# Performance work log

Hardware: AMD Instinct MI355X
Metric: run time of the kernel (lower is better)

Reference implementation:

```python
import jax, jax.numpy as jnp
import numpy as np

N_NODES = 50000
N_EDGES = 800000
D = 128


def setup_inputs() -> dict:
    key = jax.random.key(0)
    k1, k2, k3, k4 = jax.random.split(key, 4)
    x = jax.random.normal(k1, (N_NODES, D), dtype=jnp.float32)
    # nn.Linear(in, out, bias=False) weight: [out, in]
    W = jax.random.normal(k2, (D, D), dtype=jnp.float32) / np.sqrt(D)
    src = jax.random.randint(k3, (N_EDGES,), 0, N_NODES, dtype=jnp.int64)
    dst = jax.random.randint(k4, (N_EDGES,), 0, N_NODES, dtype=jnp.int64)
    return {"x": x, "W": W, "src": src, "dst": dst}


def reference(x, W, src, dst):
    # copy_src + reduce_sum: sum incoming neighbor features per destination node
    agg = jax.ops.segment_sum(x[src], dst, num_segments=N_NODES)  # [N, D]
    h = agg @ W.T                      # linear, no bias
    h = jax.nn.relu(h)                 # dropout is identity in eval mode
    h = h + x                          # residual (is_normalize=False)
    return h
```

## Files before the change

### kernel.cpp

```cpp
#include <hip/hip_runtime.h>

#define N_NODES 50000
#define N_EDGES 800000
#define D 128

#define P1_BLOCKS 64
#define P1_GRID   512
#define EDGES_PER_BLOCK (N_EDGES / P1_BLOCKS)
#define EPB_ITERS 13
#define BIN_NODES 32
#define N_BINS 1564
#define CHUNK_CAP 31
#define CELL_WORDS 32
#define LIST_CAP 48
#define RS 136

#define WS_WB16   0
#define WS_SORTED 8192
#define WS_XBF16  3211264
#define WS_END_SORT ((size_t)(WS_XBF16 + 3200000) * 4)

#define NB_SCAN ((N_NODES + 255) / 256)
#define WS_CNT     0
#define WS_ROWPTR  50000
#define WS_BSUMS   100352
#define WS_SRCS    100608
#define WS_END_CSR ((size_t)(WS_SRCS + N_EDGES) * 4)

using bf16x8 = __attribute__((ext_vector_type(8))) short;
using f32x4  = __attribute__((ext_vector_type(4))) float;

__device__ __forceinline__ unsigned bf16rne(float f) {
    unsigned b = __float_as_uint(f);
    return (b + 0x7fffu + ((b >> 16) & 1u)) >> 16;
}

__device__ __forceinline__ uint4 pack8(float4 a, float4 b) {
    uint4 o;
    o.x = bf16rne(a.x) | (bf16rne(a.y) << 16);
    o.y = bf16rne(a.z) | (bf16rne(a.w) << 16);
    o.z = bf16rne(b.x) | (bf16rne(b.y) << 16);
    o.w = bf16rne(b.z) | (bf16rne(b.w) << 16);
    return o;
}

__global__ __launch_bounds__(1024) void p1_convert_partition_kernel(
    const float* __restrict__ x, const float* __restrict__ W,
    const int* __restrict__ src, const int* __restrict__ dst,
    uint4* __restrict__ xb, uint4* __restrict__ wb,
    unsigned* __restrict__ sorted)
{
    const int tid = threadIdx.x;
    const int bid = blockIdx.x;

    if (bid >= P1_BLOCKS) {
        const int gid = (bid - P1_BLOCKS) * 1024 + tid;
        const int stride = (P1_GRID - P1_BLOCKS) * 1024;
        const float4* x4 = (const float4*)x;
        for (int i = gid; i < (N_NODES * D) / 8; i += stride)
            xb[i] = pack8(x4[2 * i], x4[2 * i + 1]);
        const float4* W4 = (const float4*)W;
        for (int i = gid; i < (D * D) / 8; i += stride)
            wb[i] = pack8(W4[2 * i], W4[2 * i + 1]);
        return;
    }

    __shared__ int lhist[N_BINS];
    for (int b = tid; b < N_BINS; b += 1024) lhist[b] = 0;
    __syncthreads();

    const int e0 = bid * EDGES_PER_BLOCK;
    int dd[EPB_ITERS], ss[EPB_ITERS];
    #pragma unroll
    for (int k = 0; k < EPB_ITERS; ++k) {
        int i = k * 1024 + tid;
        if (i < EDGES_PER_BLOCK) {
            dd[k] = dst[e0 + i];
            ss[k] = src[e0 + i];
        } else {
            dd[k] = -1;
            ss[k] = 0;
        }
    }
    #pragma unroll
    for (int k = 0; k < EPB_ITERS; ++k) {
        int d = dd[k];
        if (d >= 0) {
            int bin = d >> 5;
            int pos = atomicAdd(&lhist[bin], 1);
            if (pos < CHUNK_CAP)
                sorted[(size_t)(bin * P1_BLOCKS + bid) * CELL_WORDS + 1 + pos] =
                    ((unsigned)(d & 31) << 16) | ((unsigned)ss[k] & 0xffffu);
        }
    }
    __syncthreads();
    for (int b = tid; b < N_BINS; b += 1024)
        sorted[(size_t)(b * P1_BLOCKS + bid) * CELL_WORDS] = (unsigned)lhist[b];
}

__device__ __forceinline__ void acc_u4(float* acc, uint4 v)
{
    acc[0] += __uint_as_float(v.x << 16);
    acc[1] += __uint_as_float(v.x & 0xffff0000u);
    acc[2] += __uint_as_float(v.y << 16);
    acc[3] += __uint_as_float(v.y & 0xffff0000u);
    acc[4] += __uint_as_float(v.z << 16);
    acc[5] += __uint_as_float(v.z & 0xffff0000u);
    acc[6] += __uint_as_float(v.w << 16);
    acc[7] += __uint_as_float(v.w & 0xffff0000u);
}

__global__ __launch_bounds__(512) void gather_gemm_kernel(
    const uint4* __restrict__ xb, const unsigned* __restrict__ sorted,
    const unsigned short* __restrict__ Wb, float* __restrict__ out)
{
    __shared__ unsigned short list[BIN_NODES * LIST_CAP];
    __shared__ int lcnt[BIN_NODES];
    __shared__ unsigned short Ab[BIN_NODES * RS];
    const int tid = threadIdx.x;
    const int bin = blockIdx.x;
    if (tid < BIN_NODES) lcnt[tid] = 0;
    __syncthreads();

    {
        const int ch = tid >> 3;
        const int sub = tid & 7;
        const unsigned* base = sorted + (size_t)(bin * P1_BLOCKS + ch) * CELL_WORDS;
        int cc = (int)base[0];
        if (cc > CHUNK_CAP) cc = CHUNK_CAP;
        for (int i = sub; i < cc; i += 8) {
            unsigned p = base[1 + i];
            int dl = p >> 16;
            int pos = atomicAdd(&lcnt[dl], 1);
            if (pos < LIST_CAP) list[dl * LIST_CAP + pos] = (unsigned short)(p & 0xffffu);
        }
    }
    __syncthreads();

    {
        const int nl = tid >> 4;
        const int lane = tid & 15;
        int cc = lcnt[nl];
        if (cc > LIST_CAP) cc = LIST_CAP;
        const unsigned short* bk = &list[nl * LIST_CAP];

        float acc[8];
        #pragma unroll
        for (int i = 0; i < 8; ++i) acc[i] = 0.f;
        int e = 0;
        for (; e + 8 <= cc; e += 8) {
            uint4 v[8];
            #pragma unroll
            for (int j = 0; j < 8; ++j) v[j] = xb[(int)bk[e + j] * 16 + lane];
            #pragma unroll
            for (int j = 0; j < 8; ++j) acc_u4(acc, v[j]);
        }
        for (; e + 4 <= cc; e += 4) {
            uint4 v0 = xb[(int)bk[e] * 16 + lane];
            uint4 v1 = xb[(int)bk[e + 1] * 16 + lane];
            uint4 v2 = xb[(int)bk[e + 2] * 16 + lane];
            uint4 v3 = xb[(int)bk[e + 3] * 16 + lane];
            acc_u4(acc, v0); acc_u4(acc, v1); acc_u4(acc, v2); acc_u4(acc, v3);
        }
        for (; e < cc; ++e) acc_u4(acc, xb[(int)bk[e] * 16 + lane]);

        unsigned short* arow = &Ab[nl * RS + lane * 8];
        #pragma unroll
        for (int i = 0; i < 8; ++i) arow[i] = (unsigned short)bf16rne(acc[i]);
    }
    __syncthreads();

    const int wv = tid >> 6;
    const int lane64 = tid & 63;
    const int m = lane64 & 15;
    const int quad = lane64 >> 4;
    const int rt = wv >> 2;

    bf16x8 afrag[4];
    #pragma unroll
    for (int s = 0; s < 4; ++s)
        afrag[s] = *(const bf16x8*)(&Ab[(rt * 16 + m) * RS + quad * 8 + s * 32]);

    const unsigned short* xbs = (const unsigned short*)xb;

    #pragma unroll
    for (int half = 0; half < 2; ++half) {
        const int ct = (wv & 3) * 2 + half;
        f32x4 acc = {0.f, 0.f, 0.f, 0.f};
        const unsigned short* wrow = Wb + (size_t)(ct * 16 + m) * D + quad * 8;
        #pragma unroll
        for (int s = 0; s < 4; ++s) {
            bf16x8 bfrag = *(const bf16x8*)(wrow + s * 32);
            acc = __builtin_amdgcn_mfma_f32_16x16x32_bf16(afrag[s], bfrag, acc, 0, 0, 0);
        }
        const int cc2 = ct * 16 + m;
        #pragma unroll
        for (int r = 0; r < 4; ++r) {
            int rr = bin * BIN_NODES + rt * 16 + quad * 4 + r;
            if (rr < N_NODES) {
                float xf = __uint_as_float((unsigned)xbs[(size_t)rr * D + cc2] << 16);
                out[(size_t)rr * D + cc2] = fmaxf(acc[r], 0.f) + xf;
            }
        }
    }
}

__global__ __launch_bounds__(256) void hist_kernel(
    const int* __restrict__ dst, int* __restrict__ cnt)
{
    int e = blockIdx.x * 256 + threadIdx.x;
    if (e < N_EDGES) atomicAdd(&cnt[dst[e]], 1);
}

__device__ __forceinline__ int block_excl_scan_256(int v, int* wsums)
{
    const int lane = threadIdx.x & 63;
    const int wid = threadIdx.x >> 6;
    int incl = v;
    #pragma unroll
    for (int off = 1; off < 64; off <<= 1) {
        int t = __shfl_up(incl, off, 64);
        if (lane >= off) incl += t;
    }
    if (lane == 63) wsums[wid] = incl;
    __syncthreads();
    if (threadIdx.x == 0) {
        int s = 0;
        #pragma unroll
        for (int w = 0; w < 4; ++w) { int t = wsums[w]; wsums[w] = s; s += t; }
    }
    __syncthreads();
    return wsums[wid] + incl - v;
}

__global__ __launch_bounds__(256) void scan_reduce_kernel(
    const int* __restrict__ cnt, int* __restrict__ bsums)
{
    __shared__ int wsums[4];
    int i = blockIdx.x * 256 + threadIdx.x;
    int v = (i < N_NODES) ? cnt[i] : 0;
    const int lane = threadIdx.x & 63;
    int s = v;
    #pragma unroll
    for (int off = 32; off >= 1; off >>= 1) s += __shfl_down(s, off, 64);
    if (lane == 0) wsums[threadIdx.x >> 6] = s;
    __syncthreads();
    if (threadIdx.x == 0)
        bsums[blockIdx.x] = wsums[0] + wsums[1] + wsums[2] + wsums[3];
}

__global__ __launch_bounds__(256) void scan_bsums_kernel(
    int* __restrict__ bsums, int* __restrict__ row_ptr)
{
    __shared__ int wsums[4];
    int t = threadIdx.x;
    int v = (t < NB_SCAN) ? bsums[t] : 0;
    int excl = block_excl_scan_256(v, wsums);
    if (t < NB_SCAN) bsums[t] = excl;
    if (t == 255) row_ptr[N_NODES] = excl + v;
}

__global__ __launch_bounds__(256) void scan_final_kernel(
    int* __restrict__ cnt, const int* __restrict__ bsums,
    int* __restrict__ row_ptr)
{
    __shared__ int wsums[4];
    int i = blockIdx.x * 256 + threadIdx.x;
    int v = (i < N_NODES) ? cnt[i] : 0;
    int excl = block_excl_scan_256(v, wsums) + bsums[blockIdx.x];
    if (i < N_NODES) { row_ptr[i] = excl; cnt[i] = excl; }
}

__global__ __launch_bounds__(256) void csr_scatter_kernel(
    const int* __restrict__ src, const int* __restrict__ dst,
    int* __restrict__ cursor, int* __restrict__ srcs)
{
    int e = blockIdx.x * 256 + threadIdx.x;
    if (e < N_EDGES) {
        int pos = atomicAdd(&cursor[dst[e]], 1);
        srcs[pos] = src[e];
    }
}

__global__ __launch_bounds__(256) void gather_kernel(
    const float* __restrict__ x, const int* __restrict__ row_ptr,
    const int* __restrict__ srcs, float* __restrict__ agg)
{
    int gid = blockIdx.x * 256 + threadIdx.x;
    int node = gid >> 5;
    int lane = gid & 31;
    if (node >= N_NODES) return;
    int e = row_ptr[node];
    const int e_end = row_ptr[node + 1];
    const float4* x4 = (const float4*)x;
    float4 acc = make_float4(0.f, 0.f, 0.f, 0.f);
    for (; e + 4 <= e_end; e += 4) {
        int s0 = srcs[e], s1 = srcs[e + 1], s2 = srcs[e + 2], s3 = srcs[e + 3];
        float4 v0 = x4[(size_t)s0 * 32 + lane];
        float4 v1 = x4[(size_t)s1 * 32 + lane];
        float4 v2 = x4[(size_t)s2 * 32 + lane];
        float4 v3 = x4[(size_t)s3 * 32 + lane];
        acc.x += (v0.x + v1.x) + (v2.x + v3.x);
        acc.y += (v0.y + v1.y) + (v2.y + v3.y);
        acc.z += (v0.z + v1.z) + (v2.z + v3.z);
        acc.w += (v0.w + v1.w) + (v2.w + v3.w);
    }
    for (; e < e_end; ++e) {
        float4 v = x4[(size_t)srcs[e] * 32 + lane];
        acc.x += v.x; acc.y += v.y; acc.z += v.z; acc.w += v.w;
    }
    ((float4*)agg)[(size_t)node * 32 + lane] = acc;
}

__global__ __launch_bounds__(256) void scatter_add_kernel(
    const float* __restrict__ x, const int* __restrict__ src,
    const int* __restrict__ dst, float* __restrict__ agg)
{
    int gid = blockIdx.x * 256 + threadIdx.x;
    int edge = gid >> 5;
    int lane = gid & 31;
    if (edge >= N_EDGES) return;
    int s = src[edge];
    int d = dst[edge];
    const float4 v = *(const float4*)(x + (size_t)s * D + lane * 4);
    float* a = agg + (size_t)d * D + lane * 4;
    atomicAdd(a + 0, v.x);
    atomicAdd(a + 1, v.y);
    atomicAdd(a + 2, v.z);
    atomicAdd(a + 3, v.w);
}

#define G_ROWS 64

__global__ __launch_bounds__(256) void gemm_relu_res_kernel(
    float* __restrict__ agg, const float* __restrict__ W,
    const float* __restrict__ x)
{
    __shared__ float Wl[64 * 128];
    __shared__ float Al[G_ROWS * 128];

    const int tid = threadIdx.x;
    const int row0 = blockIdx.x * G_ROWS;

    for (int i = tid; i < G_ROWS * 32; i += 256) {
        int r = i >> 5;
        int c4 = (i & 31) << 2;
        int gr = row0 + r;
        float4 v = make_float4(0.f, 0.f, 0.f, 0.f);
        if (gr < N_NODES) v = *(const float4*)(agg + (size_t)gr * D + c4);
        *(float4*)(Al + r * 128 + c4) = v;
    }

    const int cg = tid & 31;
    const int rg = tid >> 5;
    const int c0 = cg << 2;
    const int r0 = rg << 3;

    float acc[8][4];
    #pragma unroll
    for (int i = 0; i < 8; ++i)
        #pragma unroll
        for (int j = 0; j < 4; ++j) acc[i][j] = 0.f;

    for (int h = 0; h < 2; ++h) {
        __syncthreads();
        for (int i = tid; i < 64 * 128; i += 256) {
            int c = i >> 6, kk = i & 63;
            int c_swz = (((c >> 2) ^ (kk & 31)) << 2) | (c & 3);
            Wl[kk * 128 + c_swz] = W[c * 128 + h * 64 + kk];
        }
        __syncthreads();

        for (int kc = 0; kc < 64; kc += 4) {
            float a[8][4];
            #pragma unroll
            for (int i = 0; i < 8; ++i) {
                float4 t = *(const float4*)(&Al[(r0 + i) * 128 + h * 64 + kc]);
                a[i][0] = t.x; a[i][1] = t.y; a[i][2] = t.z; a[i][3] = t.w;
            }
            #pragma unroll
            for (int j = 0; j < 4; ++j) {
                int kk = kc + j;
                const float4 wv =
                    *(const float4*)(&Wl[kk * 128 + ((cg ^ (kk & 31)) << 2)]);
                #pragma unroll
                for (int i = 0; i < 8; ++i) {
                    acc[i][0] = fmaf(a[i][j], wv.x, acc[i][0]);
                    acc[i][1] = fmaf(a[i][j], wv.y, acc[i][1]);
                    acc[i][2] = fmaf(a[i][j], wv.z, acc[i][2]);
                    acc[i][3] = fmaf(a[i][j], wv.w, acc[i][3]);
                }
            }
        }
    }

    #pragma unroll
    for (int i = 0; i < 8; ++i) {
        int gr = row0 + r0 + i;
        if (gr >= N_NODES) continue;
        const float4 xv = *(const float4*)(x + (size_t)gr * D + c0);
        float4 o;
        o.x = fmaxf(acc[i][0], 0.f) + xv.x;
        o.y = fmaxf(acc[i][1], 0.f) + xv.y;
        o.z = fmaxf(acc[i][2], 0.f) + xv.z;
        o.w = fmaxf(acc[i][3], 0.f) + xv.w;
        *(float4*)(agg + (size_t)gr * D + c0) = o;
    }
}

extern "C" void kernel_launch(void* const* d_in, const int* in_sizes, int n_in,
                              void* d_out, int out_size, void* d_ws, size_t ws_size,
                              hipStream_t stream) {
    const float* x  = (const float*)d_in[0];
    const float* W  = (const float*)d_in[1];
    const int*  src = (const int*)d_in[2];
    const int*  dst = (const int*)d_in[3];
    float* agg = (float*)d_out;

    const int eb = (N_EDGES + 255) / 256;
    int* ws = (int*)d_ws;

    if (ws_size >= WS_END_SORT) {
        uint4*    wb     = (uint4*)(ws + WS_WB16);
        unsigned* sorted = (unsigned*)(ws + WS_SORTED);
        uint4*    xb     = (uint4*)(ws + WS_XBF16);

        p1_convert_partition_kernel<<<P1_GRID, 1024, 0, stream>>>(
            x, W, src, dst, xb, wb, sorted);
        gather_gemm_kernel<<<N_BINS, 512, 0, stream>>>(
            xb, sorted, (const unsigned short*)wb, (float*)d_out);
    } else if (ws_size >= WS_END_CSR) {
        int* cnt     = ws + WS_CNT;
        int* row_ptr = ws + WS_ROWPTR;
        int* bsums   = ws + WS_BSUMS;
        int* srcs    = ws + WS_SRCS;

        hipMemsetAsync(cnt, 0, (size_t)N_NODES * sizeof(int), stream);
        hist_kernel<<<eb, 256, 0, stream>>>(dst, cnt);
        scan_reduce_kernel<<<NB_SCAN, 256, 0, stream>>>(cnt, bsums);
        scan_bsums_kernel<<<1, 256, 0, stream>>>(bsums, row_ptr);
        scan_final_kernel<<<NB_SCAN, 256, 0, stream>>>(cnt, bsums, row_ptr);
        csr_scatter_kernel<<<eb, 256, 0, stream>>>(src, dst, cnt, srcs);
        int total = N_NODES * 32;
        gather_kernel<<<(total + 255) / 256, 256, 0, stream>>>(x, row_ptr, srcs, agg);
        gemm_relu_res_kernel<<<(N_NODES + G_ROWS - 1) / G_ROWS, 256, 0, stream>>>(agg, W, x);
    } else {
        hipMemsetAsync(agg, 0, (size_t)N_NODES * D * sizeof(float), stream);
        int total = N_EDGES * 32;
        scatter_add_kernel<<<(total + 255) / 256, 256, 0, stream>>>(x, src, dst, agg);
        gemm_relu_res_kernel<<<(N_NODES + G_ROWS - 1) / G_ROWS, 256, 0, stream>>>(agg, W, x);
    }
}
```

Measured before the change: 142.0 us.

## Prefetch residual rows into LDS, vectorize bucket reads, software-pipeline gather loop

```diff
diff --git a/kernel.cpp b/kernel.cpp
--- a/kernel.cpp
+++ b/kernel.cpp
@@ -117,8 +117,16 @@
     __shared__ unsigned short list[BIN_NODES * LIST_CAP];
     __shared__ int lcnt[BIN_NODES];
     __shared__ unsigned short Ab[BIN_NODES * RS];
+    __shared__ unsigned short Res[BIN_NODES * RS];
     const int tid = threadIdx.x;
     const int bin = blockIdx.x;
+
+    uint4 resv = {0u, 0u, 0u, 0u};
+    {
+        int gi = bin * (BIN_NODES * 16) + tid;
+        if (gi < (N_NODES * D) / 8) resv = xb[gi];
+    }
+
     if (tid < BIN_NODES) lcnt[tid] = 0;
     __syncthreads();
 
@@ -128,12 +136,26 @@
         const unsigned* base = sorted + (size_t)(bin * P1_BLOCKS + ch) * CELL_WORDS;
         int cc = (int)base[0];
         if (cc > CHUNK_CAP) cc = CHUNK_CAP;
-        for (int i = sub; i < cc; i += 8) {
-            unsigned p = base[1 + i];
-            int dl = p >> 16;
-            int pos = atomicAdd(&lcnt[dl], 1);
-            if (pos < LIST_CAP) list[dl * LIST_CAP + pos] = (unsigned short)(p & 0xffffu);
-        }
+        uint4 w = ((const uint4*)base)[sub];
+        unsigned ee[4];
+        int i0, n;
+        if (sub == 0) { ee[0] = w.y; ee[1] = w.z; ee[2] = w.w; ee[3] = 0u; i0 = 0; n = 3; }
+        else          { ee[0] = w.x; ee[1] = w.y; ee[2] = w.z; ee[3] = w.w; i0 = 4 * sub - 1; n = 4; }
+        #pragma unroll
+        for (int j = 0; j < 4; ++j) {
+            if (j < n && i0 + j < cc) {
+                unsigned p = ee[j];
+                int dl = p >> 16;
+                int pos = atomicAdd(&lcnt[dl], 1);
+                if (pos < LIST_CAP) list[dl * LIST_CAP + pos] = (unsigned short)(p & 0xffffu);
+            }
+        }
+    }
+
+    {
+        const int rr = tid >> 4;
+        const int pp = tid & 15;
+        *(uint4*)&Res[rr * RS + pp * 8] = resv;
     }
     __syncthreads();
 
@@ -147,20 +169,31 @@
         float acc[8];
         #pragma unroll
         for (int i = 0; i < 8; ++i) acc[i] = 0.f;
+
         int e = 0;
-        for (; e + 8 <= cc; e += 8) {
-            uint4 v[8];
-            #pragma unroll
-            for (int j = 0; j < 8; ++j) v[j] = xb[(int)bk[e + j] * 16 + lane];
-            #pragma unroll
-            for (int j = 0; j < 8; ++j) acc_u4(acc, v[j]);
-        }
-        for (; e + 4 <= cc; e += 4) {
+        if (cc >= 8) {
+            uint4 p0 = xb[(int)bk[0] * 16 + lane];
+            uint4 p1 = xb[(int)bk[1] * 16 + lane];
+            uint4 p2 = xb[(int)bk[2] * 16 + lane];
+            uint4 p3 = xb[(int)bk[3] * 16 + lane];
+            for (; e + 8 <= cc; e += 4) {
+                uint4 q0 = xb[(int)bk[e + 4] * 16 + lane];
+                uint4 q1 = xb[(int)bk[e + 5] * 16 + lane];
+                uint4 q2 = xb[(int)bk[e + 6] * 16 + lane];
+                uint4 q3 = xb[(int)bk[e + 7] * 16 + lane];
+                acc_u4(acc, p0); acc_u4(acc, p1); acc_u4(acc, p2); acc_u4(acc, p3);
+                p0 = q0; p1 = q1; p2 = q2; p3 = q3;
+            }
+            acc_u4(acc, p0); acc_u4(acc, p1); acc_u4(acc, p2); acc_u4(acc, p3);
+            e += 4;
+        }
+        if (e + 4 <= cc) {
             uint4 v0 = xb[(int)bk[e] * 16 + lane];
             uint4 v1 = xb[(int)bk[e + 1] * 16 + lane];
             uint4 v2 = xb[(int)bk[e + 2] * 16 + lane];
             uint4 v3 = xb[(int)bk[e + 3] * 16 + lane];
             acc_u4(acc, v0); acc_u4(acc, v1); acc_u4(acc, v2); acc_u4(acc, v3);
+            e += 4;
         }
         for (; e < cc; ++e) acc_u4(acc, xb[(int)bk[e] * 16 + lane]);
 
@@ -181,8 +214,6 @@
     for (int s = 0; s < 4; ++s)
         afrag[s] = *(const bf16x8*)(&Ab[(rt * 16 + m) * RS + quad * 8 + s * 32]);
 
-    const unsigned short* xbs = (const unsigned short*)xb;
-
     #pragma unroll
     for (int half = 0; half < 2; ++half) {
         const int ct = (wv & 3) * 2 + half;
@@ -196,9 +227,10 @@
         const int cc2 = ct * 16 + m;
         #pragma unroll
         for (int r = 0; r < 4; ++r) {
-            int rr = bin * BIN_NODES + rt * 16 + quad * 4 + r;
+            int rl = rt * 16 + quad * 4 + r;
+            int rr = bin * BIN_NODES + rl;
             if (rr < N_NODES) {
-                float xf = __uint_as_float((unsigned)xbs[(size_t)rr * D + cc2] << 16);
+                float xf = __uint_as_float((unsigned)Res[rl * RS + cc2] << 16);
                 out[(size_t)rr * D + cc2] = fmaxf(acc[r], 0.f) + xf;
             }
         }
```

After: 137.2 us. 3.4% less time.
